# Kernel optimization log

Measured on AMD Instinct MI355X. Metric: run time of the kernel, lower is better.

The kernel has to match this reference:

```python
import jax, jax.numpy as jnp
import numpy as np

B, N, IN_F, OUT_F, H = 8, 1024, 128, 128, 4
HD = OUT_F // H  # 32
NEG_SLOPE = 0.2


def setup_inputs() -> dict:
    key = jax.random.key(0)
    k1, k2, k3, k4 = jax.random.split(key, 4)
    x = jax.random.normal(k1, (B, N, IN_F), dtype=jnp.float32)
    W = jax.random.normal(k2, (IN_F, OUT_F), dtype=jnp.float32) * (1.0 / np.sqrt(IN_F))
    a_src = jax.random.normal(k3, (H, HD), dtype=jnp.float32)
    a_dst = jax.random.normal(k4, (H, HD), dtype=jnp.float32)
    return {"x": x, "W": W, "a_src": a_src, "a_dst": a_dst}


def reference(x, W, a_src, a_dst):
    # Linear projection, split heads: (B, N, H, HD)
    h = (x @ W).reshape(B, N, H, HD)
    # Per-node additive attention terms: (B, N, H)
    attn_src = jnp.einsum("bnhd,hd->bnh", h, a_src)
    attn_dst = jnp.einsum("bnhd,hd->bnh", h, a_dst)
    # attn[b,i,j,h] = src_i + dst_j  -> (B, N, N, H)
    attn = attn_src[:, :, None, :] + attn_dst[:, None, :, :]
    attn = jnp.where(attn >= 0, attn, NEG_SLOPE * attn)  # LeakyReLU(0.2)
    attn = jax.nn.softmax(attn, axis=2)  # softmax over source nodes j
    # dropout is identity in eval/reference mode
    # Weighted aggregation per head: out[b,i,h,d] = sum_j attn[b,i,j,h] * h[b,j,h,d]
    out = jnp.einsum("bijh,bjhd->bihd", attn, h)
    return out.reshape(B, N, OUT_F)
```

## Files before the change

### kernel.cpp

```cpp
#include <hip/hip_runtime.h>


constexpr int CB  = 8;
constexpr int CN  = 1024;
constexpr int CF  = 128;
constexpr int CH  = 4;
constexpr int CHD = 32;
constexpr int CBH = CB * CH;
constexpr int CROWS = CB * CN;
constexpr int TROWS = CN + 1;

__global__ __launch_bounds__(256) void proj_kernel(
    const float* __restrict__ x, const float* __restrict__ W,
    const float* __restrict__ a_src, const float* __restrict__ a_dst,
    float* __restrict__ h_ws, float* __restrict__ sarr, float* __restrict__ darr)
{
    __shared__ float xs[16 * 132];
    __shared__ float wslab[64 * 128];

    const int tid = threadIdx.x, row0 = blockIdx.x * 16;

    const float4* x4 = (const float4*)x;
    #pragma unroll
    for (int m = 0; m < 2; ++m) {
        const int idx = m * 256 + tid;
        const int r = idx >> 5, k4 = idx & 31;
        *(float4*)(xs + r * 132 + k4 * 4) = x4[(size_t)row0 * 32 + idx];
    }

    const int row = tid & 15, g = tid >> 4;
    const int head = g >> 2, dd0 = (g & 3) * 8;
    float acc[8] = {0.f,0.f,0.f,0.f,0.f,0.f,0.f,0.f};

    const float4* W4 = (const float4*)W;
    for (int slab = 0; slab < 2; ++slab) {
        __syncthreads();
        #pragma unroll
        for (int m = 0; m < 8; ++m) {
            const int idx = m * 256 + tid;
            const int kk = idx >> 5, k4 = idx & 31;
            *(float4*)(wslab + kk * 128 + k4 * 4) = W4[(size_t)(slab * 64 + kk) * 32 + k4];
        }
        __syncthreads();
        #pragma unroll 4
        for (int k4 = 0; k4 < 16; ++k4) {
            const float4 xv = *(const float4*)(xs + row * 132 + slab * 64 + k4 * 4);
            const float xq[4] = {xv.x, xv.y, xv.z, xv.w};
            #pragma unroll
            for (int q = 0; q < 4; ++q) {
                const int kk = k4 * 4 + q;
                const float4 wa = *(const float4*)(wslab + kk * 128 + g * 8);
                const float4 wb = *(const float4*)(wslab + kk * 128 + g * 8 + 4);
                const float xk = xq[q];
                acc[0] += xk * wa.x; acc[1] += xk * wa.y;
                acc[2] += xk * wa.z; acc[3] += xk * wa.w;
                acc[4] += xk * wb.x; acc[5] += xk * wb.y;
                acc[6] += xk * wb.z; acc[7] += xk * wb.w;
            }
        }
    }

    const float4 as0 = *(const float4*)(a_src + head * CHD + dd0);
    const float4 as1 = *(const float4*)(a_src + head * CHD + dd0 + 4);
    const float4 ad0 = *(const float4*)(a_dst + head * CHD + dd0);
    const float4 ad1 = *(const float4*)(a_dst + head * CHD + dd0 + 4);
    float sp = acc[0]*as0.x + acc[1]*as0.y + acc[2]*as0.z + acc[3]*as0.w
             + acc[4]*as1.x + acc[5]*as1.y + acc[6]*as1.z + acc[7]*as1.w;
    float dp = acc[0]*ad0.x + acc[1]*ad0.y + acc[2]*ad0.z + acc[3]*ad0.w
             + acc[4]*ad1.x + acc[5]*ad1.y + acc[6]*ad1.z + acc[7]*ad1.w;
    sp += __shfl_xor(sp, 16); sp += __shfl_xor(sp, 32);
    dp += __shfl_xor(dp, 16); dp += __shfl_xor(dp, 32);

    const int rowg = row0 + row, b = rowg >> 10, n = rowg & 1023;
    const int bh = b * CH + head;
    float* hp = h_ws + (size_t)(bh * CN + n) * CHD + dd0;
    *(float4*)hp       = make_float4(acc[0], acc[1], acc[2], acc[3]);
    *(float4*)(hp + 4) = make_float4(acc[4], acc[5], acc[6], acc[7]);
    if ((g & 3) == 0) {
        sarr[bh * CN + n] = sp;
        darr[bh * CN + n] = dp;
    }
}

__global__ __launch_bounds__(1024) void sort_kernel(
    const float* __restrict__ darr, float* __restrict__ dsrt_g,
    int* __restrict__ pj_g, float* __restrict__ sPB_g, float* __restrict__ sSF_g,
    float* __restrict__ tbl_g)
{
    __shared__ float dsS[CN];
    __shared__ int   pjS[CN];
    const int bh = blockIdx.x, tid = threadIdx.x;

    float d = darr[bh * CN + tid];
    int   p = tid;
    for (int k = 2; k <= CN; k <<= 1) {
        for (int j = k >> 1; j > 0; j >>= 1) {
            float pd; int pp;
            if (j >= 64) {
                dsS[tid] = d; pjS[tid] = p;
                __syncthreads();
                pd = dsS[tid ^ j]; pp = pjS[tid ^ j];
                __syncthreads();
            } else {
                pd = __shfl_xor(d, j);
                pp = __shfl_xor(p, j);
            }
            const bool up = ((tid & k) == 0), low = ((tid & j) == 0);
            const bool mg = (d > pd) || (d == pd && p > pp);
            if (mg == (low == up)) { d = pd; p = pp; }
        }
    }
    dsrt_g[bh * CN + tid] = d;
    pj_g[bh * CN + tid]   = p;
    if (tid < 64) tbl_g[(size_t)bh * TROWS * 64 + (size_t)CN * 64 + tid] = 0.f;
    if (tid == 0) { sPB_g[bh * TROWS + CN] = 0.f; sSF_g[bh * TROWS + CN] = 0.f; }
}

__global__ __launch_bounds__(256) void scan_kernel(
    const float* __restrict__ h_ws, const float* __restrict__ dsrt_g,
    const int* __restrict__ pj_g, float* __restrict__ tbl_g,
    float* __restrict__ sPB_g, float* __restrict__ sSF_g,
    float* __restrict__ ctF_g, float* __restrict__ ctB_g,
    float* __restrict__ ctSF_g, float* __restrict__ ctSB_g)
{
    __shared__ float dch[128];
    __shared__ int   pch[128];
    const int bh = blockIdx.x & 31, cg = blockIdx.x >> 5;
    const int tid = threadIdx.x, base = cg * 128;

    if (tid < 128) dch[tid] = dsrt_g[bh * CN + base + tid];
    else           pch[tid - 128] = pj_g[bh * CN + base + (tid - 128)];
    __syncthreads();

    const int dir = tid >> 7, cidx = (tid >> 5) & 3, dd = tid & 31;
    const int c = cg * 4 + cidx, lb = cidx * 32;
    const float* hb = h_ws + (size_t)bh * CN * CHD;
    float* tbl = tbl_g + (size_t)bh * TROWS * 64;

    if (dir == 0) {
        float accF = 0.f, accS = 0.f;
        for (int bt = 0; bt < 2; ++bt) {
            float hv[16], dv[16];
            #pragma unroll
            for (int t = 0; t < 16; ++t) {
                const int lp = lb + bt * 16 + t;
                hv[t] = hb[(size_t)pch[lp] * CHD + dd];
                dv[t] = dch[lp];
            }
            #pragma unroll
            for (int t = 0; t < 16; ++t) {
                const int pos = base + lb + bt * 16 + t;
                const float cf = __expf(0.2f * dv[t]);
                tbl[pos * 64 + dd] = accF;
                if (dd == 0) sPB_g[bh * TROWS + pos] = accS;
                accF += cf * hv[t];
                accS += cf;
            }
        }
        ctF_g[(bh * 32 + c) * 32 + dd] = accF;
        if (dd == 0) ctSF_g[bh * 32 + c] = accS;
    } else {
        float accB = 0.f, accS = 0.f;
        for (int bt = 0; bt < 2; ++bt) {
            float hv[16], dv[16];
            #pragma unroll
            for (int t = 0; t < 16; ++t) {
                const int lp = lb + 31 - (bt * 16 + t);
                hv[t] = hb[(size_t)pch[lp] * CHD + dd];
                dv[t] = dch[lp];
            }
            #pragma unroll
            for (int t = 0; t < 16; ++t) {
                const int pos = base + lb + 31 - (bt * 16 + t);
                const float cf = __expf(dv[t]);
                accB += cf * hv[t];
                accS += cf;
                tbl[pos * 64 + 32 + dd] = accB;
                if (dd == 0) sSF_g[bh * TROWS + pos] = accS;
            }
        }
        ctB_g[(bh * 32 + c) * 32 + dd] = accB;
        if (dd == 0) ctSB_g[bh * 32 + c] = accS;
    }
}

__global__ __launch_bounds__(256) void out_kernel(
    const float* __restrict__ sarr, const float* __restrict__ dsrt_g,
    const float* __restrict__ sPB_g, const float* __restrict__ sSF_g,
    const float* __restrict__ ctF_g, const float* __restrict__ ctB_g,
    const float* __restrict__ ctSF_g, const float* __restrict__ ctSB_g,
    const float* __restrict__ tbl_g, float* __restrict__ out)
{
    __shared__ float dsS[CN];
    __shared__ float ctF[32 * 32], ctB[32 * 32];
    __shared__ float ctSF[32], ctSB[32];
    __shared__ float ofF[33 * 32], ofB[33 * 32];
    __shared__ float ofSF[33], ofSB[33];

    const int bh = blockIdx.x & 31, q = blockIdx.x >> 5;
    const int tid = threadIdx.x;

    #pragma unroll
    for (int r = 0; r < 4; ++r) {
        const int idx = r * 256 + tid;
        dsS[idx] = dsrt_g[bh * CN + idx];
        ctF[idx] = ctF_g[bh * 1024 + idx];
        ctB[idx] = ctB_g[bh * 1024 + idx];
    }
    if (tid < 32)       ctSF[tid] = ctSF_g[bh * 32 + tid];
    else if (tid < 64)  ctSB[tid - 32] = ctSB_g[bh * 32 + (tid - 32)];
    __syncthreads();

    if (tid < 32) {
        float run = 0.f;
        for (int c = 0; c < 32; ++c) { ofF[c * 32 + tid] = run; run += ctF[c * 32 + tid]; }
        ofF[32 * 32 + tid] = run;
    } else if (tid < 64) {
        const int dd = tid - 32;
        float run = 0.f;
        ofB[32 * 32 + dd] = 0.f;
        for (int c = 31; c >= 0; --c) { ofB[c * 32 + dd] = run; run += ctB[c * 32 + dd]; }
    } else if (tid == 64) {
        float run = 0.f;
        for (int c = 0; c < 32; ++c) { ofSF[c] = run; run += ctSF[c]; }
        ofSF[32] = run;
    } else if (tid == 65) {
        float run = 0.f;
        ofSB[32] = 0.f;
        for (int c = 31; c >= 0; --c) { ofSB[c] = run; run += ctSB[c]; }
    }
    __syncthreads();

    const int i = q * 256 + tid;
    const float s = sarr[bh * CN + i];
    const float c1 = __expf(s), c2v = __expf(0.2f * s), thr = -s;
    int lo = 0, hi = CN;
    while (lo < hi) { const int mid = (lo + hi) >> 1; if (dsS[mid] < thr) lo = mid + 1; else hi = mid; }
    const int k = lo, kc = k >> 5;

    const float PBs = sPB_g[bh * TROWS + k] + ofSF[kc];
    const float SFs = sSF_g[bh * TROWS + k] + ofSB[kc];
    const float inv = 1.0f / (c2v * PBs + c1 * SFs);

    const float4* tr = (const float4*)(tbl_g + (size_t)bh * TROWS * 64 + (size_t)k * 64);
    const int b = bh >> 2, hh = bh & 3;
    float4* o = (float4*)(out + (size_t)(b * CN + i) * CF + hh * 32);
    #pragma unroll
    for (int qq = 0; qq < 8; ++qq) {
        const float4 pb = tr[qq], sf = tr[8 + qq];
        const float4 oa = *(const float4*)(&ofF[kc * 32 + qq * 4]);
        const float4 ob = *(const float4*)(&ofB[kc * 32 + qq * 4]);
        float4 r;
        r.x = (c2v * (pb.x + oa.x) + c1 * (sf.x + ob.x)) * inv;
        r.y = (c2v * (pb.y + oa.y) + c1 * (sf.y + ob.y)) * inv;
        r.z = (c2v * (pb.z + oa.z) + c1 * (sf.z + ob.z)) * inv;
        r.w = (c2v * (pb.w + oa.w) + c1 * (sf.w + ob.w)) * inv;
        o[qq] = r;
    }
}

extern "C" void kernel_launch(void* const* d_in, const int* in_sizes, int n_in,
                              void* d_out, int out_size, void* d_ws, size_t ws_size,
                              hipStream_t stream) {
    const float* x     = (const float*)d_in[0];
    const float* W     = (const float*)d_in[1];
    const float* a_src = (const float*)d_in[2];
    const float* a_dst = (const float*)d_in[3];
    float* out = (float*)d_out;

    char* ws = (char*)d_ws;
    size_t off = 0;
    float* h_ws = (float*)(ws + off); off += (size_t)CROWS * CF * 4;
    float* sarr = (float*)(ws + off); off += (size_t)CBH * CN * 4;
    float* darr = (float*)(ws + off); off += (size_t)CBH * CN * 4;
    float* tblg = (float*)(ws + off); off += (size_t)CBH * TROWS * 64 * 4;
    float* dsrt = (float*)(ws + off); off += (size_t)CBH * CN * 4;
    int*   pjg  = (int*)  (ws + off); off += (size_t)CBH * CN * 4;
    float* sPBg = (float*)(ws + off); off += (size_t)CBH * TROWS * 4;
    float* sSFg = (float*)(ws + off); off += (size_t)CBH * TROWS * 4;
    float* ctFg = (float*)(ws + off); off += (size_t)CBH * 32 * 32 * 4;
    float* ctBg = (float*)(ws + off); off += (size_t)CBH * 32 * 32 * 4;
    float* ctSFg= (float*)(ws + off); off += (size_t)CBH * 32 * 4;
    float* ctSBg= (float*)(ws + off); off += (size_t)CBH * 32 * 4;
    (void)ws_size;

    proj_kernel<<<CROWS / 16, 256, 0, stream>>>(x, W, a_src, a_dst, h_ws, sarr, darr);
    sort_kernel<<<CBH, 1024, 0, stream>>>(darr, dsrt, pjg, sPBg, sSFg, tblg);
    scan_kernel<<<256, 256, 0, stream>>>(h_ws, dsrt, pjg, tblg, sPBg, sSFg,
                                         ctFg, ctBg, ctSFg, ctSBg);
    out_kernel<<<128, 256, 0, stream>>>(sarr, dsrt, sPBg, sSFg,
                                        ctFg, ctBg, ctSFg, ctSBg, tblg, out);
}
```

Measured before the change: 93.27 us.

## Replace bitonic sort with histogram bucket sort and in-bucket fixup

Replaces the full bitonic sort of the destination scores with a counting (bucket) sort over 1024 uniform-width bins computed from the per-head min and max. The output kernel then locates the query's bucket directly instead of binary searching, uses prefix sums at the bucket boundaries, and walks the few in-bucket elements explicitly, choosing the LeakyReLU branch per element. This is meant to remove the many barrier-bound bitonic stages. It adds a variable-length loop in the output kernel that can diverge when buckets are crowded. Separately, the projection kernel is re-tiled to 8 rows per block with 4 outputs per thread, doubling the block count.

```diff
diff --git a/kernel.cpp b/kernel.cpp
--- a/kernel.cpp
+++ b/kernel.cpp
@@ -9,28 +9,26 @@
 constexpr int CBH = CB * CH;
 constexpr int CROWS = CB * CN;
 constexpr int TROWS = CN + 1;
+constexpr int NBK = 1024;
 
 __global__ __launch_bounds__(256) void proj_kernel(
     const float* __restrict__ x, const float* __restrict__ W,
     const float* __restrict__ a_src, const float* __restrict__ a_dst,
     float* __restrict__ h_ws, float* __restrict__ sarr, float* __restrict__ darr)
 {
-    __shared__ float xs[16 * 132];
+    __shared__ float xs[8 * 132];
     __shared__ float wslab[64 * 128];
 
-    const int tid = threadIdx.x, row0 = blockIdx.x * 16;
-
-    const float4* x4 = (const float4*)x;
-    #pragma unroll
-    for (int m = 0; m < 2; ++m) {
-        const int idx = m * 256 + tid;
-        const int r = idx >> 5, k4 = idx & 31;
-        *(float4*)(xs + r * 132 + k4 * 4) = x4[(size_t)row0 * 32 + idx];
-    }
-
-    const int row = tid & 15, g = tid >> 4;
-    const int head = g >> 2, dd0 = (g & 3) * 8;
-    float acc[8] = {0.f,0.f,0.f,0.f,0.f,0.f,0.f,0.f};
+    const int tid = threadIdx.x, row0 = blockIdx.x * 8;
+
+    {
+        const int rr = tid >> 5, k4 = tid & 31;
+        *(float4*)(xs + rr * 132 + k4 * 4) = ((const float4*)x)[(size_t)row0 * 32 + tid];
+    }
+
+    const int r = tid >> 5, c4 = tid & 31;
+    const int head = c4 >> 3, dd0 = (c4 & 7) * 4;
+    float acc[4] = {0.f, 0.f, 0.f, 0.f};
 
     const float4* W4 = (const float4*)W;
     for (int slab = 0; slab < 2; ++slab) {
@@ -44,76 +42,110 @@
         __syncthreads();
         #pragma unroll 4
         for (int k4 = 0; k4 < 16; ++k4) {
-            const float4 xv = *(const float4*)(xs + row * 132 + slab * 64 + k4 * 4);
+            const float4 xv = *(const float4*)(xs + r * 132 + slab * 64 + k4 * 4);
             const float xq[4] = {xv.x, xv.y, xv.z, xv.w};
             #pragma unroll
             for (int q = 0; q < 4; ++q) {
                 const int kk = k4 * 4 + q;
-                const float4 wa = *(const float4*)(wslab + kk * 128 + g * 8);
-                const float4 wb = *(const float4*)(wslab + kk * 128 + g * 8 + 4);
+                const float4 wv = *(const float4*)(wslab + kk * 128 + c4 * 4);
                 const float xk = xq[q];
-                acc[0] += xk * wa.x; acc[1] += xk * wa.y;
-                acc[2] += xk * wa.z; acc[3] += xk * wa.w;
-                acc[4] += xk * wb.x; acc[5] += xk * wb.y;
-                acc[6] += xk * wb.z; acc[7] += xk * wb.w;
-            }
-        }
-    }
-
-    const float4 as0 = *(const float4*)(a_src + head * CHD + dd0);
-    const float4 as1 = *(const float4*)(a_src + head * CHD + dd0 + 4);
-    const float4 ad0 = *(const float4*)(a_dst + head * CHD + dd0);
-    const float4 ad1 = *(const float4*)(a_dst + head * CHD + dd0 + 4);
-    float sp = acc[0]*as0.x + acc[1]*as0.y + acc[2]*as0.z + acc[3]*as0.w
-             + acc[4]*as1.x + acc[5]*as1.y + acc[6]*as1.z + acc[7]*as1.w;
-    float dp = acc[0]*ad0.x + acc[1]*ad0.y + acc[2]*ad0.z + acc[3]*ad0.w
-             + acc[4]*ad1.x + acc[5]*ad1.y + acc[6]*ad1.z + acc[7]*ad1.w;
-    sp += __shfl_xor(sp, 16); sp += __shfl_xor(sp, 32);
-    dp += __shfl_xor(dp, 16); dp += __shfl_xor(dp, 32);
-
-    const int rowg = row0 + row, b = rowg >> 10, n = rowg & 1023;
+                acc[0] += xk * wv.x; acc[1] += xk * wv.y;
+                acc[2] += xk * wv.z; acc[3] += xk * wv.w;
+            }
+        }
+    }
+
+    const float4 as = *(const float4*)(a_src + head * CHD + dd0);
+    const float4 ad = *(const float4*)(a_dst + head * CHD + dd0);
+    float sp = acc[0]*as.x + acc[1]*as.y + acc[2]*as.z + acc[3]*as.w;
+    float dp = acc[0]*ad.x + acc[1]*ad.y + acc[2]*ad.z + acc[3]*ad.w;
+    sp += __shfl_xor(sp, 1); sp += __shfl_xor(sp, 2); sp += __shfl_xor(sp, 4);
+    dp += __shfl_xor(dp, 1); dp += __shfl_xor(dp, 2); dp += __shfl_xor(dp, 4);
+
+    const int rowg = row0 + r, b = rowg >> 10, n = rowg & 1023;
     const int bh = b * CH + head;
-    float* hp = h_ws + (size_t)(bh * CN + n) * CHD + dd0;
-    *(float4*)hp       = make_float4(acc[0], acc[1], acc[2], acc[3]);
-    *(float4*)(hp + 4) = make_float4(acc[4], acc[5], acc[6], acc[7]);
-    if ((g & 3) == 0) {
+    *(float4*)(h_ws + (size_t)(bh * CN + n) * CHD + dd0) =
+        make_float4(acc[0], acc[1], acc[2], acc[3]);
+    if ((c4 & 7) == 0) {
         sarr[bh * CN + n] = sp;
         darr[bh * CN + n] = dp;
     }
 }
 
-__global__ __launch_bounds__(1024) void sort_kernel(
+__global__ __launch_bounds__(1024) void count_kernel(
     const float* __restrict__ darr, float* __restrict__ dsrt_g,
-    int* __restrict__ pj_g, float* __restrict__ sPB_g, float* __restrict__ sSF_g,
-    float* __restrict__ tbl_g)
+    int* __restrict__ pj_g, int* __restrict__ bs_g, float* __restrict__ prm_g,
+    float* __restrict__ sPB_g, float* __restrict__ sSF_g, float* __restrict__ tbl_g)
 {
-    __shared__ float dsS[CN];
-    __shared__ int   pjS[CN];
+    __shared__ int   cnts[NBK];
+    __shared__ int   startsS[NBK];
+    __shared__ float redS[32];
+    __shared__ int   wsumS[16];
+    __shared__ float prmS[2];
+
     const int bh = blockIdx.x, tid = threadIdx.x;
-
-    float d = darr[bh * CN + tid];
-    int   p = tid;
-    for (int k = 2; k <= CN; k <<= 1) {
-        for (int j = k >> 1; j > 0; j >>= 1) {
-            float pd; int pp;
-            if (j >= 64) {
-                dsS[tid] = d; pjS[tid] = p;
-                __syncthreads();
-                pd = dsS[tid ^ j]; pp = pjS[tid ^ j];
-                __syncthreads();
-            } else {
-                pd = __shfl_xor(d, j);
-                pp = __shfl_xor(p, j);
-            }
-            const bool up = ((tid & k) == 0), low = ((tid & j) == 0);
-            const bool mg = (d > pd) || (d == pd && p > pp);
-            if (mg == (low == up)) { d = pd; p = pp; }
-        }
-    }
-    dsrt_g[bh * CN + tid] = d;
-    pj_g[bh * CN + tid]   = p;
+    const int lane = tid & 63, wid = tid >> 6;
+
+    const float d = darr[bh * CN + tid];
+
+    float mn = d, mx = d;
+    #pragma unroll
+    for (int off = 1; off < 64; off <<= 1) {
+        mn = fminf(mn, __shfl_xor(mn, off));
+        mx = fmaxf(mx, __shfl_xor(mx, off));
+    }
+    if (lane == 0) { redS[wid] = mn; redS[16 + wid] = mx; }
+    cnts[tid] = 0;
+    __syncthreads();
+    if (tid == 0) {
+        float m0 = redS[0], m1 = redS[16];
+        for (int w = 1; w < 16; ++w) { m0 = fminf(m0, redS[w]); m1 = fmaxf(m1, redS[16 + w]); }
+        const float rng = fmaxf(m1 - m0, 1e-30f);
+        const float invw = (float)NBK / rng;
+        prmS[0] = m0; prmS[1] = invw;
+        prm_g[bh * 2] = m0; prm_g[bh * 2 + 1] = invw;
+    }
+    __syncthreads();
+    const float mnb = prmS[0], invw = prmS[1];
+    const int f = (int)fminf(fmaxf((d - mnb) * invw, 0.0f), 1023.0f);
+    const int rank = atomicAdd(&cnts[f], 1);
+    __syncthreads();
+
+    const int c = cnts[tid];
+    int incl = c;
+    #pragma unroll
+    for (int off = 1; off < 64; off <<= 1) {
+        const int t = __shfl_up(incl, off);
+        if (lane >= off) incl += t;
+    }
+    if (lane == 63) wsumS[wid] = incl;
+    __syncthreads();
+    if (tid < 16) {
+        const int v = wsumS[tid];
+        int iv = v;
+        #pragma unroll
+        for (int off = 1; off < 16; off <<= 1) {
+            const int t = __shfl_up(iv, off);
+            if (tid >= off) iv += t;
+        }
+        wsumS[tid] = iv - v;
+    }
+    __syncthreads();
+    const int excl = incl - c + wsumS[wid];
+    startsS[tid] = excl;
+    bs_g[bh * (NBK + 1) + tid] = excl;
+    __syncthreads();
+
+    const int pos = startsS[f] + rank;
+    dsrt_g[bh * CN + pos] = d;
+    pj_g[bh * CN + pos]   = tid;
+
+    if (tid == 0) {
+        bs_g[bh * (NBK + 1) + NBK] = CN;
+        sPB_g[bh * TROWS + CN] = 0.f;
+        sSF_g[bh * TROWS + CN] = 0.f;
+    }
     if (tid < 64) tbl_g[(size_t)bh * TROWS * 64 + (size_t)CN * 64 + tid] = 0.f;
-    if (tid == 0) { sPB_g[bh * TROWS + CN] = 0.f; sSF_g[bh * TROWS + CN] = 0.f; }
 }
 
 __global__ __launch_bounds__(256) void scan_kernel(
@@ -185,13 +217,17 @@
 }
 
 __global__ __launch_bounds__(256) void out_kernel(
-    const float* __restrict__ sarr, const float* __restrict__ dsrt_g,
+    const float* __restrict__ h_ws, const float* __restrict__ sarr,
+    const float* __restrict__ dsrt_g, const int* __restrict__ pj_g,
+    const int* __restrict__ bs_g, const float* __restrict__ prm_g,
     const float* __restrict__ sPB_g, const float* __restrict__ sSF_g,
     const float* __restrict__ ctF_g, const float* __restrict__ ctB_g,
     const float* __restrict__ ctSF_g, const float* __restrict__ ctSB_g,
     const float* __restrict__ tbl_g, float* __restrict__ out)
 {
     __shared__ float dsS[CN];
+    __shared__ int   pjS[CN];
+    __shared__ int   bsS[NBK + 1];
     __shared__ float ctF[32 * 32], ctB[32 * 32];
     __shared__ float ctSF[32], ctSB[32];
     __shared__ float ofF[33 * 32], ofB[33 * 32];
@@ -201,12 +237,15 @@
     const int tid = threadIdx.x;
 
     #pragma unroll
-    for (int r = 0; r < 4; ++r) {
-        const int idx = r * 256 + tid;
+    for (int rr = 0; rr < 4; ++rr) {
+        const int idx = rr * 256 + tid;
         dsS[idx] = dsrt_g[bh * CN + idx];
+        pjS[idx] = pj_g[bh * CN + idx];
+        bsS[idx] = bs_g[bh * (NBK + 1) + idx];
         ctF[idx] = ctF_g[bh * 1024 + idx];
         ctB[idx] = ctB_g[bh * 1024 + idx];
     }
+    if (tid == 0) bsS[NBK] = bs_g[bh * (NBK + 1) + NBK];
     if (tid < 32)       ctSF[tid] = ctSF_g[bh * 32 + tid];
     else if (tid < 64)  ctSB[tid - 32] = ctSB_g[bh * 32 + (tid - 32)];
     __syncthreads();
@@ -234,28 +273,54 @@
     const int i = q * 256 + tid;
     const float s = sarr[bh * CN + i];
     const float c1 = __expf(s), c2v = __expf(0.2f * s), thr = -s;
-    int lo = 0, hi = CN;
-    while (lo < hi) { const int mid = (lo + hi) >> 1; if (dsS[mid] < thr) lo = mid + 1; else hi = mid; }
-    const int k = lo, kc = k >> 5;
-
-    const float PBs = sPB_g[bh * TROWS + k] + ofSF[kc];
-    const float SFs = sSF_g[bh * TROWS + k] + ofSB[kc];
-    const float inv = 1.0f / (c2v * PBs + c1 * SFs);
-
-    const float4* tr = (const float4*)(tbl_g + (size_t)bh * TROWS * 64 + (size_t)k * 64);
+    const float mnb = prm_g[bh * 2], invw = prm_g[bh * 2 + 1];
+    const int kb = (int)fminf(fmaxf((thr - mnb) * invw, 0.0f), 1023.0f);
+    const int q0 = bsS[kb], q1 = bsS[kb + 1];
+    const int kcf = q0 >> 5, kcb = q1 >> 5;
+
+    float pbs = sPB_g[bh * TROWS + q0] + ofSF[kcf];
+    float sfs = sSF_g[bh * TROWS + q1] + ofSB[kcb];
+
+    const float4* trf = (const float4*)(tbl_g + (size_t)bh * TROWS * 64 + (size_t)q0 * 64);
+    const float4* trb = (const float4*)(tbl_g + (size_t)bh * TROWS * 64 + (size_t)q1 * 64 + 32);
+    float4 vF[8], vB[8];
+    #pragma unroll
+    for (int qq = 0; qq < 8; ++qq) {
+        const float4 pb = trf[qq], oa = *(const float4*)(&ofF[kcf * 32 + qq * 4]);
+        const float4 sf = trb[qq], ob = *(const float4*)(&ofB[kcb * 32 + qq * 4]);
+        vF[qq] = make_float4(pb.x + oa.x, pb.y + oa.y, pb.z + oa.z, pb.w + oa.w);
+        vB[qq] = make_float4(sf.x + ob.x, sf.y + ob.y, sf.z + ob.z, sf.w + ob.w);
+    }
+
+    const float* hb = h_ws + (size_t)bh * CN * CHD;
+    for (int p = q0; p < q1; ++p) {
+        const float dq = dsS[p];
+        const float4* hr = (const float4*)(hb + (size_t)pjS[p] * CHD);
+        const bool pre = (dq < thr);
+        const float w = __expf(pre ? 0.2f * dq : dq);
+        if (pre) pbs += w; else sfs += w;
+        #pragma unroll
+        for (int qq = 0; qq < 8; ++qq) {
+            const float4 hv = hr[qq];
+            if (pre) {
+                vF[qq].x += w * hv.x; vF[qq].y += w * hv.y;
+                vF[qq].z += w * hv.z; vF[qq].w += w * hv.w;
+            } else {
+                vB[qq].x += w * hv.x; vB[qq].y += w * hv.y;
+                vB[qq].z += w * hv.z; vB[qq].w += w * hv.w;
+            }
+        }
+    }
+
+    const float inv = 1.0f / (c2v * pbs + c1 * sfs);
     const int b = bh >> 2, hh = bh & 3;
     float4* o = (float4*)(out + (size_t)(b * CN + i) * CF + hh * 32);
     #pragma unroll
     for (int qq = 0; qq < 8; ++qq) {
-        const float4 pb = tr[qq], sf = tr[8 + qq];
-        const float4 oa = *(const float4*)(&ofF[kc * 32 + qq * 4]);
-        const float4 ob = *(const float4*)(&ofB[kc * 32 + qq * 4]);
-        float4 r;
-        r.x = (c2v * (pb.x + oa.x) + c1 * (sf.x + ob.x)) * inv;
-        r.y = (c2v * (pb.y + oa.y) + c1 * (sf.y + ob.y)) * inv;
-        r.z = (c2v * (pb.z + oa.z) + c1 * (sf.z + ob.z)) * inv;
-        r.w = (c2v * (pb.w + oa.w) + c1 * (sf.w + ob.w)) * inv;
-        o[qq] = r;
+        o[qq] = make_float4((c2v * vF[qq].x + c1 * vB[qq].x) * inv,
+                            (c2v * vF[qq].y + c1 * vB[qq].y) * inv,
+                            (c2v * vF[qq].z + c1 * vB[qq].z) * inv,
+                            (c2v * vF[qq].w + c1 * vB[qq].w) * inv);
     }
 }
 
@@ -282,12 +347,14 @@
     float* ctBg = (float*)(ws + off); off += (size_t)CBH * 32 * 32 * 4;
     float* ctSFg= (float*)(ws + off); off += (size_t)CBH * 32 * 4;
     float* ctSBg= (float*)(ws + off); off += (size_t)CBH * 32 * 4;
+    int*   bsg  = (int*)  (ws + off); off += (size_t)CBH * (NBK + 1) * 4;
+    float* prmg = (float*)(ws + off); off += (size_t)CBH * 2 * 4;
     (void)ws_size;
 
-    proj_kernel<<<CROWS / 16, 256, 0, stream>>>(x, W, a_src, a_dst, h_ws, sarr, darr);
-    sort_kernel<<<CBH, 1024, 0, stream>>>(darr, dsrt, pjg, sPBg, sSFg, tblg);
+    proj_kernel<<<CROWS / 8, 256, 0, stream>>>(x, W, a_src, a_dst, h_ws, sarr, darr);
+    count_kernel<<<CBH, 1024, 0, stream>>>(darr, dsrt, pjg, bsg, prmg, sPBg, sSFg, tblg);
     scan_kernel<<<256, 256, 0, stream>>>(h_ws, dsrt, pjg, tblg, sPBg, sSFg,
                                          ctFg, ctBg, ctSFg, ctSBg);
-    out_kernel<<<128, 256, 0, stream>>>(sarr, dsrt, sPBg, sSFg,
-                                        ctFg, ctBg, ctSFg, ctSBg, tblg, out);
-}
+    out_kernel<<<128, 256, 0, stream>>>(h_ws, sarr, dsrt, pjg, bsg, prmg,
+                                        sPBg, sSFg, ctFg, ctBg, ctSFg, ctSBg, tblg, out);
+}
```

Result: no change. 94.23 us (median of 2 runs) (+1.0%).
